# Optimization experiments

Hardware: AMD Instinct MI355X
Metric: run time of the kernel (lower is better)

## Reference

```python
import jax, jax.numpy as jnp
import numpy as np

NUM_USER = 30000
NUM_ITEM = 30000
N = NUM_USER + NUM_ITEM
DIM = 64          # dim_latent
HID = 4 * DIM     # MLP hidden = 4*dim_latent
E_PAIRS = 500000  # user-item interactions; symmetrized -> 2*E_PAIRS edges
K = 10            # sampling (user-graph neighbors)
B = 2048          # batch_size
DV, DA, DT = 1024, 128, 100


def setup_inputs() -> dict:
    key = jax.random.key(0)
    ks = jax.random.split(key, 24)
    src = jax.random.randint(ks[0], (E_PAIRS,), 0, NUM_USER)
    dst = jax.random.randint(ks[1], (E_PAIRS,), NUM_USER, N)
    # symmetrize like torch.cat((edge, edge[[1,0]]), dim=1)
    edge_index = jnp.stack([jnp.concatenate([src, dst]),
                            jnp.concatenate([dst, src])])  # [2, 2*E_PAIRS]

    def lin_w(k, o, i):
        s = 1.0 / np.sqrt(i)
        return jax.random.uniform(k, (o, i), minval=-s, maxval=s, dtype=jnp.float32)

    return {
        "user_nodes": jax.random.randint(ks[2], (B,), 0, NUM_USER),
        "pos_item_nodes": jax.random.randint(ks[3], (B,), NUM_USER, N),
        "neg_item_nodes": jax.random.randint(ks[4], (B,), NUM_USER, N),
        "user_graph": jax.random.randint(ks[5], (NUM_USER, K), 0, NUM_USER),
        "edge_index": edge_index,
        "user_weight_matrix": jax.nn.softmax(jax.random.normal(ks[6], (NUM_USER, K), dtype=jnp.float32), axis=-1),
        "v_feat": jax.random.normal(ks[7], (NUM_ITEM, DV), dtype=jnp.float32),
        "a_feat": jax.random.normal(ks[8], (NUM_ITEM, DA), dtype=jnp.float32),
        "t_feat": jax.random.normal(ks[9], (NUM_ITEM, DT), dtype=jnp.float32),
        "v_pref": 0.1 * jax.random.normal(ks[10], (NUM_USER, DIM), dtype=jnp.float32),
        "a_pref": 0.1 * jax.random.normal(ks[11], (NUM_USER, DIM), dtype=jnp.float32),
        "t_pref": 0.1 * jax.random.normal(ks[12], (NUM_USER, DIM), dtype=jnp.float32),
        "v_W1": lin_w(ks[13], HID, DV), "v_b1": jnp.zeros((HID,), jnp.float32),
        "v_W2": lin_w(ks[14], DIM, HID), "v_b2": jnp.zeros((DIM,), jnp.float32),
        "a_W1": lin_w(ks[15], HID, DA), "a_b1": jnp.zeros((HID,), jnp.float32),
        "a_W2": lin_w(ks[16], DIM, HID), "a_b2": jnp.zeros((DIM,), jnp.float32),
        "t_W1": lin_w(ks[17], HID, DT), "t_b1": jnp.zeros((HID,), jnp.float32),
        "t_W2": lin_w(ks[18], DIM, HID), "t_b2": jnp.zeros((DIM,), jnp.float32),
        "weight_u": jax.nn.softmax(jax.random.normal(ks[19], (NUM_USER, 3, 1), dtype=jnp.float32), axis=1),
    }


def _l2norm(x):
    # F.normalize(x): rowwise L2 with eps=1e-12
    return x / jnp.maximum(jnp.linalg.norm(x, axis=-1, keepdims=True), 1e-12)


def _gcn_conv(x, src, dst, dinv):
    # Base_gcn(aggr='add'): out[i] = sum_{e: dst_e=i} dinv[src_e]*dinv[dst_e]*x[src_e]
    norm = dinv[src] * dinv[dst]
    return jax.ops.segment_sum(norm[:, None] * x[src], dst, num_segments=N)


def _modality(feat, pref, W1, b1, W2, b2, src, dst, dinv):
    # GCN.forward (Movielens branch, dim_latent=64)
    temp = jax.nn.leaky_relu(feat @ W1.T + b1) @ W2.T + b2  # MLP_1(leaky_relu(MLP(f)))
    x = _l2norm(jnp.concatenate([pref, temp], axis=0))       # [N, DIM]
    h = _gcn_conv(x, src, dst, dinv)
    h1 = _gcn_conv(h, src, dst, dinv)
    return h + x + h1


def reference(user_nodes, pos_item_nodes, neg_item_nodes, user_graph, edge_index,
              user_weight_matrix, v_feat, a_feat, t_feat,
              v_pref, a_pref, t_pref,
              v_W1, v_b1, v_W2, v_b2,
              a_W1, a_b1, a_W2, a_b2,
              t_W1, t_b1, t_W2, t_b2, weight_u):
    src, dst = edge_index[0], edge_index[1]
    deg = jax.ops.segment_sum(jnp.ones_like(src, dtype=jnp.float32), src, num_segments=N)
    dinv = jnp.where(deg > 0, deg ** -0.5, 0.0)

    v_rep = _modality(v_feat, v_pref, v_W1, v_b1, v_W2, v_b2, src, dst, dinv)
    a_rep = _modality(a_feat, a_pref, a_W1, a_b1, a_W2, a_b2, src, dst, dinv)
    t_rep = _modality(t_feat, t_pref, t_W1, t_b1, t_W2, t_b2, src, dst, dinv)

    representation = (v_rep + a_rep + t_rep) / 3.0
    # weighted_sum construction: per-user learned modality weights [U,3,1]
    user_stack = jnp.stack([v_rep[:NUM_USER], a_rep[:NUM_USER], t_rep[:NUM_USER]], axis=2)  # [U, D, 3]
    user_rep = jnp.einsum('udm,umo->ud', user_stack, weight_u)
    item_rep = representation[NUM_USER:]

    # User_Graph_sample: weighted sum over k sampled user neighbors
    h_u1 = jnp.einsum('uk,ukd->ud', user_weight_matrix, user_rep[user_graph])
    user_rep = user_rep + h_u1

    result = jnp.concatenate([user_rep, item_rep], axis=0)  # [N, DIM]
    u = result[user_nodes]
    pos_scores = jnp.sum(u * result[pos_item_nodes], axis=1)
    neg_scores = jnp.sum(u * result[neg_item_nodes], axis=1)
    return pos_scores, neg_scores
```

## Files before the change

kernel.cpp:

```cpp
#include <hip/hip_runtime.h>
#include <hip/hip_bf16.h>
#include <math.h>

#define NUSER 30000
#define NITEM 30000
#define NN    60000
#define NE    1000000
#define DIMV  64
#define XW    192
#define HIDW  256
#define NB    2048
#define KNB   10
#define MPAD  30080
#define NCH   235

typedef __attribute__((ext_vector_type(8))) short bf16x8;
typedef __attribute__((ext_vector_type(4))) float f32x4;

__device__ __forceinline__ short f2bf(float f) {
    union { float f; unsigned u; } v; v.f = f;
    unsigned r = v.u + 0x7fff + ((v.u >> 16) & 1);
    return (short)(r >> 16);
}
__device__ __forceinline__ float bflo(unsigned v) { return __int_as_float(v << 16); }
__device__ __forceinline__ float bfhi(unsigned v) { return __int_as_float(v & 0xffff0000u); }
__device__ __forceinline__ unsigned pack2(float a, float b) {
    return (unsigned)(unsigned short)f2bf(a) | ((unsigned)(unsigned short)f2bf(b) << 16);
}
__device__ __forceinline__ void async16(void* lds, const void* g) {
    __builtin_amdgcn_global_load_lds(
        (const __attribute__((address_space(1))) unsigned*)g,
        (__attribute__((address_space(3))) unsigned*)lds, 16, 0, 0);
}

__global__ void k_deg(const int* __restrict__ src, unsigned* __restrict__ deg) {
    int e = blockIdx.x * blockDim.x + threadIdx.x;
    if (e < NE) atomicAdd(&deg[src[e]], 1u);
}
__global__ void k_dinv(const unsigned* __restrict__ deg, float* __restrict__ dinv) {
    int i = blockIdx.x * blockDim.x + threadIdx.x;
    if (i < NN) { unsigned d = deg[i]; dinv[i] = d ? rsqrtf((float)d) : 0.f; }
}
__global__ __launch_bounds__(256)
void k_bsum(const unsigned* __restrict__ deg, int* __restrict__ bsum) {
    __shared__ int red[4];
    int g = blockIdx.x * 256 + threadIdx.x;
    int v = (g < NN) ? (int)deg[g] : 0;
    for (int o = 32; o > 0; o >>= 1) v += __shfl_down(v, o);
    int lane = threadIdx.x & 63, wave = threadIdx.x >> 6;
    if (lane == 0) red[wave] = v;
    __syncthreads();
    if (threadIdx.x == 0) bsum[blockIdx.x] = red[0] + red[1] + red[2] + red[3];
}
__global__ __launch_bounds__(256)
void k_bscan(const int* __restrict__ bsum, int* __restrict__ bscan) {
    __shared__ int s[256];
    int t = threadIdx.x;
    int v = (t < NCH) ? bsum[t] : 0;
    s[t] = v;
    __syncthreads();
    for (int o = 1; o < 256; o <<= 1) {
        int u = (t >= o) ? s[t - o] : 0;
        __syncthreads();
        s[t] += u;
        __syncthreads();
    }
    if (t < NCH) bscan[t] = s[t] - v;
}
__global__ __launch_bounds__(256)
void k_rowptr(const unsigned* __restrict__ deg, const int* __restrict__ bscan,
              int* __restrict__ rowptr) {
    __shared__ int s[256];
    int g = blockIdx.x * 256 + threadIdx.x, t = threadIdx.x;
    int v = (g < NN) ? (int)deg[g] : 0;
    s[t] = v;
    __syncthreads();
    for (int o = 1; o < 256; o <<= 1) {
        int u = (t >= o) ? s[t - o] : 0;
        __syncthreads();
        s[t] += u;
        __syncthreads();
    }
    int base = bscan[blockIdx.x];
    if (g < NN) rowptr[g] = base + s[t] - v;
    if (g == NN - 1) rowptr[NN] = base + s[t];
}
__global__ void k_fill(const int* __restrict__ src, const int* __restrict__ dst,
                       const float* __restrict__ dinv, const int* __restrict__ rowptr,
                       unsigned* __restrict__ cursor, int2* __restrict__ csr) {
    int e = blockIdx.x * blockDim.x + threadIdx.x;
    if (e >= NE) return;
    int s = src[e], d = dst[e];
    int pos = (int)atomicAdd(&cursor[d], 1u);
    int2 ew;
    ew.x = s;
    ew.y = __float_as_int(dinv[s] * dinv[d]);
    csr[rowptr[d] + pos] = ew;
}

struct CvtArgs { const float* src[6]; short* dst[6]; };
__constant__ __device__ const int C8PRE[7]  = {0,32768,36864,40960,43008,45056,47104};
__constant__ __device__ const int C8SH[6]   = {7,4,4,5,5,5};
__constant__ __device__ const int C8COLS[6] = {1024,128,100,256,256,256};
__constant__ __device__ const int C8ROWS[6] = {256,256,256,64,64,64};
#define CVT8_TOTAL 47104

__global__ __launch_bounds__(256)
void k_convert(CvtArgs a) {
    int cid = blockIdx.x * 256 + threadIdx.x;
    if (cid >= CVT8_TOTAL) return;
    int j = 0;
    while (cid >= C8PRE[j + 1]) ++j;
    int local = cid - C8PRE[j];
    int sh = C8SH[j];
    int r = local >> sh;
    int col = (local & ((1 << sh) - 1)) * 8;
    int cols = C8COLS[j];
    bf16x8 o = (bf16x8)0;
    if (r < C8ROWS[j]) {
        const float* s = a.src[j] + (size_t)r * cols + col;
        if (col + 8 <= cols) {
            float4 f0 = *(const float4*)s;
            float4 f1 = *(const float4*)(s + 4);
            o[0] = f2bf(f0.x); o[1] = f2bf(f0.y); o[2] = f2bf(f0.z); o[3] = f2bf(f0.w);
            o[4] = f2bf(f1.x); o[5] = f2bf(f1.y); o[6] = f2bf(f1.z); o[7] = f2bf(f1.w);
        } else {
            #pragma unroll
            for (int q = 0; q < 8; ++q)
                if (col + q < cols) o[q] = f2bf(s[q]);
        }
    }
    *(bf16x8*)(a.dst[j] + ((size_t)r << (sh + 3)) + col) = o;
}

__device__ __forceinline__ bf16x8 ldfrag(const short* lds, int row, int kbyte) {
    int off = (row * 128 + kbyte) ^ ((row & 7) << 4);
    return *(const bf16x8*)((const char*)lds + off);
}
#define STAGE_TILE(SMEM, BASEPTR, LDK, ROWOFF, K0, NITERS)                          \
    _Pragma("unroll")                                                                \
    for (int i_ = 0; i_ < (NITERS); ++i_) {                                          \
        int c_ = i_ * 256 + wave * 64 + lane;                                        \
        int r_ = c_ >> 3, slot_ = c_ & 7;                                            \
        int ss_ = slot_ ^ (r_ & 7);                                                  \
        const char* gp_ = (const char*)((BASEPTR) + (size_t)((ROWOFF) + r_) * (LDK)  \
                                        + (K0)) + ss_ * 16;                          \
        async16(&(SMEM)[(i_ * 256 + wave * 64) * 8], gp_);                           \
    }

struct G1Args { const float* A[3]; const short* W[3]; const float* bias[3];
                short* C[3]; int K[3]; int Ksrc[3]; };
__global__ __launch_bounds__(256)
void gemm1_mfma(G1Args g) {
    __shared__ __align__(16) short sA[128 * 64];
    __shared__ __align__(16) short sB[256 * 64];
    int m = blockIdx.z;
    int K  = g.K[m];
    int Ks = g.Ksrc[m];
    const float* A = g.A[m];
    const short* W = g.W[m];
    int lane = threadIdx.x & 63, wave = threadIdx.x >> 6;
    int wr = wave >> 1, wc = wave & 1;
    int lane15 = lane & 15, lhi = lane >> 4;
    int row0 = blockIdx.x * 128;
    int srow = threadIdx.x >> 1, shalf = threadIdx.x & 1;
    int grow = row0 + srow;
    bool rowok = grow < NITEM;
    const float* arow = A + (size_t)grow * Ks + shalf * 32;
    f32x4 acc[4][8] = {};
    for (int t = 0; t < (K >> 6); ++t) {
        int k0 = t * 64;
        float4 f[8];
        int gk = k0 + shalf * 32;
        if (rowok && gk + 32 <= Ks) {
            #pragma unroll
            for (int q = 0; q < 8; ++q) f[q] = *(const float4*)(arow + k0 + q * 4);
        } else {
            #pragma unroll
            for (int q = 0; q < 8; ++q) {
                float4 z = make_float4(0.f, 0.f, 0.f, 0.f);
                if (rowok) {
                    int c = gk + q * 4;
                    if (c + 4 <= Ks) {
                        z = *(const float4*)(arow + k0 + q * 4);
                    } else {
                        if (c + 0 < Ks) z.x = arow[k0 + q * 4 + 0];
                        if (c + 1 < Ks) z.y = arow[k0 + q * 4 + 1];
                        if (c + 2 < Ks) z.z = arow[k0 + q * 4 + 2];
                        if (c + 3 < Ks) z.w = arow[k0 + q * 4 + 3];
                    }
                }
                f[q] = z;
            }
        }
        #pragma unroll
        for (int q = 0; q < 4; ++q) {
            bf16x8 o;
            float4 lo = f[q * 2], hi = f[q * 2 + 1];
            o[0] = f2bf(lo.x); o[1] = f2bf(lo.y); o[2] = f2bf(lo.z); o[3] = f2bf(lo.w);
            o[4] = f2bf(hi.x); o[5] = f2bf(hi.y); o[6] = f2bf(hi.z); o[7] = f2bf(hi.w);
            int c8 = shalf * 4 + q;
            int off = (srow * 128 + c8 * 16) ^ ((srow & 7) << 4);
            *(bf16x8*)((char*)sA + off) = o;
        }
        STAGE_TILE(sB, W, K, 0, k0, 8)
        __syncthreads();
        #pragma unroll
        for (int ks = 0; ks < 2; ++ks) {
            int kb = ks * 64 + lhi * 16;
            bf16x8 a[4], b[8];
            #pragma unroll
            for (int mi = 0; mi < 4; ++mi) a[mi] = ldfrag(sA, wr * 64 + mi * 16 + lane15, kb);
            #pragma unroll
            for (int ni = 0; ni < 8; ++ni) b[ni] = ldfrag(sB, wc * 128 + ni * 16 + lane15, kb);
            #pragma unroll
            for (int mi = 0; mi < 4; ++mi)
                #pragma unroll
                for (int ni = 0; ni < 8; ++ni)
                    acc[mi][ni] = __builtin_amdgcn_mfma_f32_16x16x32_bf16(a[mi], b[ni], acc[mi][ni], 0, 0, 0);
        }
        __syncthreads();
    }
    short* C = g.C[m];
    const float* bias = g.bias[m];
    #pragma unroll
    for (int mi = 0; mi < 4; ++mi) {
        int grow0 = row0 + wr * 64 + mi * 16 + lhi * 4;
        #pragma unroll
        for (int ni = 0; ni < 8; ++ni) {
            int gcol = wc * 128 + ni * 16 + lane15;
            float bv = bias[gcol];
            #pragma unroll
            for (int r = 0; r < 4; ++r) {
                float v = acc[mi][ni][r] + bv;
                v = v > 0.f ? v : 0.01f * v;
                C[(size_t)(grow0 + r) * HIDW + gcol] = f2bf(v);
            }
        }
    }
}

struct G2Args { const short* A[3]; const short* W[3]; const float* bias[3]; };
__global__ __launch_bounds__(256)
void gemm2_mfma(G2Args g, float* __restrict__ X, short* __restrict__ Xb) {
    __shared__ __align__(16) short sA[128 * 64];
    __shared__ __align__(16) short sB[64 * 64];
    int m = blockIdx.z;
    const short* A = g.A[m];
    const short* W = g.W[m];
    int lane = threadIdx.x & 63, wave = threadIdx.x >> 6;
    int lane15 = lane & 15, lhi = lane >> 4;
    int row0 = blockIdx.x * 128;
    const int K = HIDW;
    f32x4 acc[2][4] = {};
    for (int t = 0; t < 4; ++t) {
        int k0 = t * 64;
        STAGE_TILE(sA, A, K, row0, k0, 4)
        STAGE_TILE(sB, W, K, 0, k0, 2)
        __syncthreads();
        #pragma unroll
        for (int ks = 0; ks < 2; ++ks) {
            int kb = ks * 64 + lhi * 16;
            bf16x8 a[2], b[4];
            #pragma unroll
            for (int mi = 0; mi < 2; ++mi) a[mi] = ldfrag(sA, wave * 32 + mi * 16 + lane15, kb);
            #pragma unroll
            for (int ni = 0; ni < 4; ++ni) b[ni] = ldfrag(sB, ni * 16 + lane15, kb);
            #pragma unroll
            for (int mi = 0; mi < 2; ++mi)
                #pragma unroll
                for (int ni = 0; ni < 4; ++ni)
                    acc[mi][ni] = __builtin_amdgcn_mfma_f32_16x16x32_bf16(a[mi], b[ni], acc[mi][ni], 0, 0, 0);
        }
        __syncthreads();
    }
    const float* bias = g.bias[m];
    #pragma unroll
    for (int mi = 0; mi < 2; ++mi) {
        float v[4][4];
        float sumsq[4] = {};
        #pragma unroll
        for (int ni = 0; ni < 4; ++ni) {
            float bv = bias[ni * 16 + lane15];
            #pragma unroll
            for (int r = 0; r < 4; ++r) {
                float x = acc[mi][ni][r] + bv;
                v[ni][r] = x;
                sumsq[r] += x * x;
            }
        }
        #pragma unroll
        for (int r = 0; r < 4; ++r) {
            float s = sumsq[r];
            s += __shfl_xor(s, 1); s += __shfl_xor(s, 2);
            s += __shfl_xor(s, 4); s += __shfl_xor(s, 8);
            sumsq[r] = 1.f / fmaxf(sqrtf(s), 1e-12f);
        }
        int grow0 = row0 + wave * 32 + mi * 16 + lhi * 4;
        #pragma unroll
        for (int r = 0; r < 4; ++r) {
            int grow = grow0 + r;
            if (grow < NITEM) {
                float sc = sumsq[r];
                size_t o = (size_t)(NUSER + grow) * XW + m * DIMV;
                #pragma unroll
                for (int ni = 0; ni < 4; ++ni) {
                    float val = v[ni][r] * sc;
                    X[o + ni * 16 + lane15] = val;
                    Xb[o + ni * 16 + lane15] = f2bf(val);
                }
            }
        }
    }
}

__global__ void k_users_norm(const float* __restrict__ vp, const float* __restrict__ ap,
                             const float* __restrict__ tp, float* __restrict__ X,
                             short* __restrict__ Xb) {
    int gw = (blockIdx.x * blockDim.x + threadIdx.x) >> 6;
    int lane = threadIdx.x & 63;
    if (gw >= NUSER * 3) return;
    int u = gw / 3, m = gw % 3;
    const float* p = (m == 0) ? vp : (m == 1) ? ap : tp;
    float v = p[(size_t)u * DIMV + lane];
    float s = v * v;
    for (int o = 32; o > 0; o >>= 1) s += __shfl_xor(s, o);
    float sc = 1.f / fmaxf(sqrtf(s), 1e-12f);
    size_t o = (size_t)u * XW + m * DIMV + lane;
    float val = v * sc;
    X[o] = val;
    Xb[o] = f2bf(val);
}

template<int MODE>
__global__ __launch_bounds__(256)
void k_spmm(const int* __restrict__ rowptr, const int2* __restrict__ csr,
            const short* __restrict__ INB, const float* __restrict__ Xf,
            float* __restrict__ OUTf, short* __restrict__ OUTB) {
    int n = blockIdx.x * 4 + (threadIdx.x >> 6);
    int l = threadIdx.x & 63;
    if (n >= NN) return;
    int lo = rowptr[n], hi = rowptr[n + 1];
    int lc = l < 48 ? l : 47;
    float f0 = 0.f, f1 = 0.f, f2 = 0.f, f3 = 0.f;
    for (int base = lo; base < hi; base += 64) {
        int idx = base + l;
        int2 e = (idx < hi) ? csr[idx] : make_int2(0, 0);
        int m = hi - base; if (m > 64) m = 64;
        int j = 0;
        for (; j + 4 <= m; j += 4) {
            int s0 = __builtin_amdgcn_readlane(e.x, j + 0);
            int s1 = __builtin_amdgcn_readlane(e.x, j + 1);
            int s2 = __builtin_amdgcn_readlane(e.x, j + 2);
            int s3 = __builtin_amdgcn_readlane(e.x, j + 3);
            float w0 = __int_as_float(__builtin_amdgcn_readlane(e.y, j + 0));
            float w1 = __int_as_float(__builtin_amdgcn_readlane(e.y, j + 1));
            float w2 = __int_as_float(__builtin_amdgcn_readlane(e.y, j + 2));
            float w3 = __int_as_float(__builtin_amdgcn_readlane(e.y, j + 3));
            uint2 v0 = ((const uint2*)(INB + (size_t)s0 * XW))[lc];
            uint2 v1 = ((const uint2*)(INB + (size_t)s1 * XW))[lc];
            uint2 v2 = ((const uint2*)(INB + (size_t)s2 * XW))[lc];
            uint2 v3 = ((const uint2*)(INB + (size_t)s3 * XW))[lc];
            f0 += w0 * bflo(v0.x); f1 += w0 * bfhi(v0.x);
            f2 += w0 * bflo(v0.y); f3 += w0 * bfhi(v0.y);
            f0 += w1 * bflo(v1.x); f1 += w1 * bfhi(v1.x);
            f2 += w1 * bflo(v1.y); f3 += w1 * bfhi(v1.y);
            f0 += w2 * bflo(v2.x); f1 += w2 * bfhi(v2.x);
            f2 += w2 * bflo(v2.y); f3 += w2 * bfhi(v2.y);
            f0 += w3 * bflo(v3.x); f1 += w3 * bfhi(v3.x);
            f2 += w3 * bflo(v3.y); f3 += w3 * bfhi(v3.y);
        }
        for (; j < m; ++j) {
            int s0 = __builtin_amdgcn_readlane(e.x, j);
            float w0 = __int_as_float(__builtin_amdgcn_readlane(e.y, j));
            uint2 v0 = ((const uint2*)(INB + (size_t)s0 * XW))[lc];
            f0 += w0 * bflo(v0.x); f1 += w0 * bfhi(v0.x);
            f2 += w0 * bflo(v0.y); f3 += w0 * bfhi(v0.y);
        }
    }
    if (MODE == 1) {
        float4 xv = ((const float4*)(Xf + (size_t)n * XW))[lc];
        uint2 hb = ((const uint2*)(INB + (size_t)n * XW))[lc];
        f0 += xv.x + bflo(hb.x); f1 += xv.y + bfhi(hb.x);
        f2 += xv.z + bflo(hb.y); f3 += xv.w + bfhi(hb.y);
    }
    if (l < 48) {
        if (MODE == 0) {
            uint2 ob;
            ob.x = pack2(f0, f1);
            ob.y = pack2(f2, f3);
            ((uint2*)(OUTB + (size_t)n * XW))[l] = ob;
        } else {
            ((float4*)(OUTf + (size_t)n * XW))[l] = make_float4(f0, f1, f2, f3);
        }
    }
}

__global__ void k_combine(const float* __restrict__ REP, const float* __restrict__ wu,
                          float* __restrict__ UR, float* __restrict__ RES) {
    int t = blockIdx.x * blockDim.x + threadIdx.x;
    if (t >= NN * DIMV) return;
    int n = t >> 6, d = t & 63;
    const float* r = REP + (size_t)n * XW;
    float r0 = r[d], r1 = r[DIMV + d], r2 = r[2 * DIMV + d];
    if (n < NUSER) {
        float w0 = wu[n * 3 + 0], w1 = wu[n * 3 + 1], w2 = wu[n * 3 + 2];
        UR[(size_t)n * DIMV + d] = r0 * w0 + r1 * w1 + r2 * w2;
    } else {
        RES[(size_t)n * DIMV + d] = (r0 + r1 + r2) * (1.f / 3.f);
    }
}
__global__ void k_usergraph(const float* __restrict__ UR, const int* __restrict__ g,
                            const float* __restrict__ w, float* __restrict__ RES) {
    int t = blockIdx.x * blockDim.x + threadIdx.x;
    if (t >= NUSER * DIMV) return;
    int n = t >> 6, d = t & 63;
    float acc = UR[(size_t)n * DIMV + d];
    for (int k = 0; k < KNB; ++k) {
        int nb = g[n * KNB + k];
        acc += w[n * KNB + k] * UR[(size_t)nb * DIMV + d];
    }
    RES[(size_t)n * DIMV + d] = acc;
}
__global__ void k_scores(const float* __restrict__ RES, const int* __restrict__ un,
                         const int* __restrict__ pn, const int* __restrict__ nn,
                         float* __restrict__ out) {
    int gw = (blockIdx.x * blockDim.x + threadIdx.x) >> 6;
    int lane = threadIdx.x & 63;
    if (gw >= NB) return;
    int u = un[gw], p = pn[gw], ng = nn[gw];
    float uv = RES[(size_t)u * DIMV + lane];
    float ps = uv * RES[(size_t)p * DIMV + lane];
    float ns = uv * RES[(size_t)ng * DIMV + lane];
    for (int o = 32; o > 0; o >>= 1) {
        ps += __shfl_xor(ps, o);
        ns += __shfl_xor(ns, o);
    }
    if (lane == 0) { out[gw] = ps; out[NB + gw] = ns; }
}

extern "C" void kernel_launch(void* const* d_in, const int* in_sizes, int n_in,
                              void* d_out, int out_size, void* d_ws, size_t ws_size,
                              hipStream_t stream) {
    const int*   un    = (const int*)d_in[0];
    const int*   pn    = (const int*)d_in[1];
    const int*   ngn   = (const int*)d_in[2];
    const int*   ug    = (const int*)d_in[3];
    const int*   eidx  = (const int*)d_in[4];
    const float* uwm   = (const float*)d_in[5];
    const float* feats[3] = { (const float*)d_in[6], (const float*)d_in[7], (const float*)d_in[8] };
    const float* prefs[3] = { (const float*)d_in[9], (const float*)d_in[10], (const float*)d_in[11] };
    const float* W1[3] = { (const float*)d_in[12], (const float*)d_in[16], (const float*)d_in[20] };
    const float* b1[3] = { (const float*)d_in[13], (const float*)d_in[17], (const float*)d_in[21] };
    const float* W2[3] = { (const float*)d_in[14], (const float*)d_in[18], (const float*)d_in[22] };
    const float* b2[3] = { (const float*)d_in[15], (const float*)d_in[19], (const float*)d_in[23] };
    const float* wu    = (const float*)d_in[24];
    float* out = (float*)d_out;

    const int* esrc = eidx;
    const int* edst = eidx + NE;

    char* ws = (char*)d_ws;
    size_t off = 0;
    auto alloc = [&](size_t bytes) { void* p = ws + off; off = (off + bytes + 255) & ~(size_t)255; return p; };
    unsigned* deg    = (unsigned*)alloc(NN * 4);
    float*    dinv   = (float*)alloc(NN * 4);
    int*      rowptr = (int*)alloc((NN + 1) * 4);
    int*      bsum   = (int*)alloc(NCH * 4);
    int*      bscan  = (int*)alloc(NCH * 4);
    int2*     csr    = (int2*)alloc((size_t)NE * 8);
    float*    X      = (float*)alloc((size_t)NN * XW * 4);
    short*    Xb     = (short*)alloc((size_t)NN * XW * 2);
    char* region2 = (char*)alloc((size_t)3 * MPAD * HIDW * 2);
    short* hid[3] = { (short*)region2,
                      (short*)(region2 + (size_t)MPAD * HIDW * 2),
                      (short*)(region2 + (size_t)2 * MPAD * HIDW * 2) };
    float* RES = (float*)region2;
    float* UR  = (float*)(region2 + (size_t)NN * DIMV * 4 + 40960);
    short* Hb  = (short*)(region2 + (size_t)NN * DIMV * 4 + 40960 + (size_t)NUSER * DIMV * 4);
    short* w1b = (short*)alloc((size_t)256 * 1280 * 2);
    short* w1s[3] = { w1b, w1b + 256 * 1024, w1b + 256 * (1024 + 128) };
    short* w2b = (short*)alloc((size_t)3 * 64 * HIDW * 2);
    short* w2s[3] = { w2b, w2b + 64 * HIDW, w2b + 2 * 64 * HIDW };

    CvtArgs ca;
    ca.src[0] = W1[0]; ca.src[1] = W1[1]; ca.src[2] = W1[2];
    ca.src[3] = W2[0]; ca.src[4] = W2[1]; ca.src[5] = W2[2];
    ca.dst[0] = w1s[0]; ca.dst[1] = w1s[1]; ca.dst[2] = w1s[2];
    ca.dst[3] = w2s[0]; ca.dst[4] = w2s[1]; ca.dst[5] = w2s[2];
    k_convert<<<(CVT8_TOTAL + 255) / 256, 256, 0, stream>>>(ca);

    hipMemsetAsync(deg, 0, NN * 4, stream);
    k_deg<<<(NE + 255) / 256, 256, 0, stream>>>(esrc, deg);
    k_dinv<<<(NN + 255) / 256, 256, 0, stream>>>(deg, dinv);
    k_bsum<<<NCH, 256, 0, stream>>>(deg, bsum);
    k_bscan<<<1, 256, 0, stream>>>(bsum, bscan);
    k_rowptr<<<NCH, 256, 0, stream>>>(deg, bscan, rowptr);
    hipMemsetAsync(deg, 0, NN * 4, stream);
    k_fill<<<(NE + 255) / 256, 256, 0, stream>>>(esrc, edst, dinv, rowptr, deg, csr);

    G1Args g1;
    for (int m = 0; m < 3; ++m) { g1.bias[m] = b1[m]; g1.C[m] = hid[m]; g1.W[m] = w1s[m]; g1.A[m] = feats[m]; }
    g1.K[0] = 1024; g1.K[1] = 128; g1.K[2] = 128;
    g1.Ksrc[0] = 1024; g1.Ksrc[1] = 128; g1.Ksrc[2] = 100;
    gemm1_mfma<<<dim3(MPAD / 128, 1, 3), 256, 0, stream>>>(g1);

    G2Args g2;
    for (int m = 0; m < 3; ++m) { g2.A[m] = hid[m]; g2.W[m] = w2s[m]; g2.bias[m] = b2[m]; }
    gemm2_mfma<<<dim3(MPAD / 128, 1, 3), 256, 0, stream>>>(g2, X, Xb);
    k_users_norm<<<(NUSER * 3 * 64 + 255) / 256, 256, 0, stream>>>(prefs[0], prefs[1], prefs[2], X, Xb);

    k_spmm<0><<<(NN + 3) / 4, 256, 0, stream>>>(rowptr, csr, Xb, nullptr, nullptr, Hb);

    k_spmm<1><<<(NN + 3) / 4, 256, 0, stream>>>(rowptr, csr, Hb, X, X, nullptr);

    k_combine<<<(NN * DIMV + 255) / 256, 256, 0, stream>>>(X, wu, UR, RES);
    k_usergraph<<<(NUSER * DIMV + 255) / 256, 256, 0, stream>>>(UR, ug, uwm, RES);
    k_scores<<<(NB * 64 + 255) / 256, 256, 0, stream>>>(RES, un, pn, ngn, out);
}
```

Baseline: 348.6 us.

## Drop LDS staging in first MLP GEMM, load fragments directly from global

The first-layer GEMM no longer stages A and W tiles through shared memory with barriers. Each wave now loads its bf16 W fragments and fp32 A rows straight from global memory, converting A to bf16 in registers, and feeds the MFMAs directly. The block tile shrinks from 128 to 64 rows, doubling the grid, and output stores gain a row bound check. This removes LDS traffic and synchronisation but gives up cross-wave reuse, so W is re-read from global/L2 by every wave with uncoalesced 16-byte accesses.

```diff
diff --git a/kernel.cpp b/kernel.cpp
--- a/kernel.cpp
+++ b/kernel.cpp
@@ -150,91 +150,76 @@
 
 struct G1Args { const float* A[3]; const short* W[3]; const float* bias[3];
                 short* C[3]; int K[3]; int Ksrc[3]; };
+
+__device__ __forceinline__ bf16x8 ldcvtA(const float* ap, int kk, int Ks, bool ok) {
+    bf16x8 o;
+    if (ok && kk + 8 <= Ks) {
+        float4 x = *(const float4*)(ap + kk);
+        float4 y = *(const float4*)(ap + kk + 4);
+        o[0] = f2bf(x.x); o[1] = f2bf(x.y); o[2] = f2bf(x.z); o[3] = f2bf(x.w);
+        o[4] = f2bf(y.x); o[5] = f2bf(y.y); o[6] = f2bf(y.z); o[7] = f2bf(y.w);
+    } else {
+        #pragma unroll
+        for (int j = 0; j < 8; ++j) {
+            float v = (ok && kk + j < Ks) ? ap[kk + j] : 0.f;
+            o[j] = f2bf(v);
+        }
+    }
+    return o;
+}
+
 __global__ __launch_bounds__(256)
 void gemm1_mfma(G1Args g) {
-    __shared__ __align__(16) short sA[128 * 64];
-    __shared__ __align__(16) short sB[256 * 64];
     int m = blockIdx.z;
     int K  = g.K[m];
     int Ks = g.Ksrc[m];
     const float* A = g.A[m];
     const short* W = g.W[m];
-    int lane = threadIdx.x & 63, wave = threadIdx.x >> 6;
-    int wr = wave >> 1, wc = wave & 1;
+    int tid = threadIdx.x;
+    int lane = tid & 63, wave = tid >> 6;
     int lane15 = lane & 15, lhi = lane >> 4;
-    int row0 = blockIdx.x * 128;
-    int srow = threadIdx.x >> 1, shalf = threadIdx.x & 1;
-    int grow = row0 + srow;
-    bool rowok = grow < NITEM;
-    const float* arow = A + (size_t)grow * Ks + shalf * 32;
-    f32x4 acc[4][8] = {};
-    for (int t = 0; t < (K >> 6); ++t) {
-        int k0 = t * 64;
-        float4 f[8];
-        int gk = k0 + shalf * 32;
-        if (rowok && gk + 32 <= Ks) {
-            #pragma unroll
-            for (int q = 0; q < 8; ++q) f[q] = *(const float4*)(arow + k0 + q * 4);
-        } else {
-            #pragma unroll
-            for (int q = 0; q < 8; ++q) {
-                float4 z = make_float4(0.f, 0.f, 0.f, 0.f);
-                if (rowok) {
-                    int c = gk + q * 4;
-                    if (c + 4 <= Ks) {
-                        z = *(const float4*)(arow + k0 + q * 4);
-                    } else {
-                        if (c + 0 < Ks) z.x = arow[k0 + q * 4 + 0];
-                        if (c + 1 < Ks) z.y = arow[k0 + q * 4 + 1];
-                        if (c + 2 < Ks) z.z = arow[k0 + q * 4 + 2];
-                        if (c + 3 < Ks) z.w = arow[k0 + q * 4 + 3];
-                    }
-                }
-                f[q] = z;
-            }
-        }
-        #pragma unroll
-        for (int q = 0; q < 4; ++q) {
-            bf16x8 o;
-            float4 lo = f[q * 2], hi = f[q * 2 + 1];
-            o[0] = f2bf(lo.x); o[1] = f2bf(lo.y); o[2] = f2bf(lo.z); o[3] = f2bf(lo.w);
-            o[4] = f2bf(hi.x); o[5] = f2bf(hi.y); o[6] = f2bf(hi.z); o[7] = f2bf(hi.w);
-            int c8 = shalf * 4 + q;
-            int off = (srow * 128 + c8 * 16) ^ ((srow & 7) << 4);
-            *(bf16x8*)((char*)sA + off) = o;
-        }
-        STAGE_TILE(sB, W, K, 0, k0, 8)
-        __syncthreads();
-        #pragma unroll
-        for (int ks = 0; ks < 2; ++ks) {
-            int kb = ks * 64 + lhi * 16;
-            bf16x8 a[4], b[8];
-            #pragma unroll
-            for (int mi = 0; mi < 4; ++mi) a[mi] = ldfrag(sA, wr * 64 + mi * 16 + lane15, kb);
-            #pragma unroll
-            for (int ni = 0; ni < 8; ++ni) b[ni] = ldfrag(sB, wc * 128 + ni * 16 + lane15, kb);
-            #pragma unroll
-            for (int mi = 0; mi < 4; ++mi)
-                #pragma unroll
-                for (int ni = 0; ni < 8; ++ni)
-                    acc[mi][ni] = __builtin_amdgcn_mfma_f32_16x16x32_bf16(a[mi], b[ni], acc[mi][ni], 0, 0, 0);
-        }
-        __syncthreads();
+    int wrow = wave & 1, wcol = wave >> 1;
+    int row0 = blockIdx.x * 64 + wrow * 32;
+    int cbase = wcol * 128;
+    int r0 = row0 + lane15, r1 = row0 + 16 + lane15;
+    bool ok0 = r0 < NITEM, ok1 = r1 < NITEM;
+    const float* ap0 = A + (size_t)(ok0 ? r0 : 0) * Ks;
+    const float* ap1 = A + (size_t)(ok1 ? r1 : 0) * Ks;
+    const short* bp = W + (size_t)(cbase + lane15) * K + lhi * 8;
+    int kA = lhi * 8;
+    f32x4 acc[2][8] = {};
+    #pragma unroll 4
+    for (int k0 = 0; k0 < K; k0 += 32) {
+        bf16x8 b[8];
+        #pragma unroll
+        for (int ni = 0; ni < 8; ++ni)
+            b[ni] = *(const bf16x8*)(bp + (size_t)ni * 16 * K + k0);
+        int kk = k0 + kA;
+        bf16x8 a0 = ldcvtA(ap0, kk, Ks, ok0);
+        bf16x8 a1 = ldcvtA(ap1, kk, Ks, ok1);
+        #pragma unroll
+        for (int ni = 0; ni < 8; ++ni) {
+            acc[0][ni] = __builtin_amdgcn_mfma_f32_16x16x32_bf16(a0, b[ni], acc[0][ni], 0, 0, 0);
+            acc[1][ni] = __builtin_amdgcn_mfma_f32_16x16x32_bf16(a1, b[ni], acc[1][ni], 0, 0, 0);
+        }
     }
     short* C = g.C[m];
     const float* bias = g.bias[m];
     #pragma unroll
-    for (int mi = 0; mi < 4; ++mi) {
-        int grow0 = row0 + wr * 64 + mi * 16 + lhi * 4;
+    for (int mi = 0; mi < 2; ++mi) {
+        int gr0 = row0 + mi * 16 + lhi * 4;
         #pragma unroll
         for (int ni = 0; ni < 8; ++ni) {
-            int gcol = wc * 128 + ni * 16 + lane15;
+            int gcol = cbase + ni * 16 + lane15;
             float bv = bias[gcol];
             #pragma unroll
             for (int r = 0; r < 4; ++r) {
-                float v = acc[mi][ni][r] + bv;
-                v = v > 0.f ? v : 0.01f * v;
-                C[(size_t)(grow0 + r) * HIDW + gcol] = f2bf(v);
+                int grow = gr0 + r;
+                if (grow < NITEM) {
+                    float v = acc[mi][ni][r] + bv;
+                    v = v > 0.f ? v : 0.01f * v;
+                    C[(size_t)grow * HIDW + gcol] = f2bf(v);
+                }
             }
         }
     }
@@ -503,7 +488,7 @@
     for (int m = 0; m < 3; ++m) { g1.bias[m] = b1[m]; g1.C[m] = hid[m]; g1.W[m] = w1s[m]; g1.A[m] = feats[m]; }
     g1.K[0] = 1024; g1.K[1] = 128; g1.K[2] = 128;
     g1.Ksrc[0] = 1024; g1.Ksrc[1] = 128; g1.Ksrc[2] = 100;
-    gemm1_mfma<<<dim3(MPAD / 128, 1, 3), 256, 0, stream>>>(g1);
+    gemm1_mfma<<<dim3(MPAD / 64, 1, 3), 256, 0, stream>>>(g1);
 
     G2Args g2;
     for (int m = 0; m < 3; ++m) { g2.A[m] = hid[m]; g2.W[m] = w2s[m]; g2.bias[m] = b2[m]; }
```

Measured after the change: 404.0 us. 1.16x slower.
